# Performance work log

Measured on AMD Instinct MI355X. Metric: run time of the kernel, lower is better.

The kernel has to match this reference:

```python
import jax, jax.numpy as jnp
import numpy as np
from jax import lax

# config (matches init_kwargs)
HEADS = 4
KD2 = 256          # key_dim // 2
KNN = 16
BLOCK = 128        # knn * block_rate
COL = 512          # value_size // block
VALUE_SIZE = 65536 # key_num ** 2
D_OUT = 512
D_IN = 1024
QUERYDIM = HEADS * KD2  # 1024
KERNEL = 3


def setup_inputs() -> dict:
    key = jax.random.key(0)
    ks = jax.random.split(key, 8)
    B, T = 2, 2048
    return {
        "x": jax.random.normal(ks[0], (B, T, D_IN), dtype=jnp.float32),
        "conv_w": jax.random.normal(ks[1], (D_IN, 1, KERNEL), dtype=jnp.float32) * 0.1,
        "conv_b": jax.random.normal(ks[2], (D_IN,), dtype=jnp.float32) * 0.1,
        "lin_w": jax.random.normal(ks[3], (QUERYDIM, D_IN), dtype=jnp.float32) * (D_IN ** -0.5),
        "lin_b": jax.random.normal(ks[4], (QUERYDIM,), dtype=jnp.float32) * 0.1,
        "rowkeys": jax.random.normal(ks[5], (BLOCK, HEADS, KD2), dtype=jnp.float32) * (KD2 ** -0.5),
        "colkeys": jax.random.normal(ks[6], (COL, HEADS, KD2), dtype=jnp.float32) * (KD2 ** -0.5),
        "value_w": jax.random.normal(ks[7], (VALUE_SIZE, D_OUT), dtype=jnp.float32),
    }


def _forward(x, conv_w, conv_b, lin_w, lin_b, rowkeys, colkeys, value_w):
    B, T, C = x.shape
    # --- Querynet: causal depthwise conv1d + linear ---
    xt = jnp.transpose(x, (0, 2, 1))  # (B, C, T)
    y = lax.conv_general_dilated(
        xt, conv_w, window_strides=(1,), padding=[(KERNEL - 1, 0)],
        feature_group_count=C, dimension_numbers=("NCH", "OIH", "NCH"))
    y = y + conv_b[None, :, None]
    y = jnp.transpose(y, (0, 2, 1))                     # (B, T, C)
    query = y @ lin_w.T + lin_b                         # (B, T, querydim)
    # torch: query.view(B, heads, T, key_dim//2) -- raw C-order reshape
    q = query.reshape(B, HEADS, T, KD2)
    # --- block_wise_choice.get_indices ---
    score = jnp.einsum("bhtd,ehd->bhte", q, rowkeys)    # (B,H,T,block)
    col_scores = jnp.einsum("bhtd,chd->bhtc", q, colkeys)  # (B,H,T,col)
    score_col, idx_col = lax.top_k(col_scores, 1)       # (B,H,T,1)
    base = jnp.arange(BLOCK, dtype=jnp.int32)
    indices = base[None, None, None, :] * COL + idx_col  # (B,H,T,block)
    score = score + score_col                            # broadcast add
    # torch .view(B,H,-1,T): raw C-order reshape mixing tokens and blocks
    score = score.reshape(B, HEADS, BLOCK, T)
    indices = indices.reshape(B, HEADS, BLOCK, T)
    k = T * KNN // BLOCK
    score_top, dispatch = lax.top_k(score, k)            # (B,H,block,k), sorted desc
    idx_top = jnp.take_along_axis(indices, dispatch, axis=-1)
    score_r = score_top.reshape(B, BLOCK, -1)            # (B, block, H*k)
    idx_r = idx_top.reshape(B, BLOCK, -1)
    disp_r = dispatch.reshape(B, BLOCK, -1)
    # --- Memory_value: gather-weight-scatter ---
    gathered = value_w[idx_r]                            # (B, block, H*k, d)
    weighted = (gathered * score_r[..., None]).reshape(B, -1, D_OUT)
    flat_disp = disp_r.reshape(B, -1)                    # values in [0, T)
    out = jnp.zeros((B, T, D_OUT), dtype=weighted.dtype)
    out = out.at[jnp.arange(B)[:, None], flat_disp].add(weighted)
    return out


def reference(x, conv_w, conv_b, lin_w, lin_b, rowkeys, colkeys, value_w):
    return _forward(x, conv_w, conv_b, lin_w, lin_b, rowkeys, colkeys, value_w)
```

## Files before the change

### kernel.cpp

```cpp
#include <hip/hip_runtime.h>

constexpr int Bc   = 2;
constexpr int Tc   = 2048;
constexpr int Cc   = 1024;
constexpr int QDc  = 1024;
constexpr int Hc   = 4;
constexpr int KD2c = 256;
constexpr int BLKc = 128;
constexpr int COLc = 512;
constexpr int DOUTc= 512;
constexpr int KSELc= 256;
constexpr int NKEYS= BLKc + COLc;
constexpr int NBINS= Bc * Tc;
constexpr int NSEL = Bc * Hc * BLKc * KSELc;

typedef short bf16x8 __attribute__((ext_vector_type(8)));
typedef float f32x4  __attribute__((ext_vector_type(4)));

__device__ __forceinline__ unsigned short f2bf(float f) {
    unsigned u = __float_as_uint(f);
    u += 0x7FFFu + ((u >> 16) & 1u);
    return (unsigned short)(u >> 16);
}
__device__ __forceinline__ float bf2f(unsigned short h) {
    return __uint_as_float((unsigned)h << 16);
}
__device__ __forceinline__ void splitbf3(float f, unsigned short* h,
                                         unsigned short* m, unsigned short* l) {
    unsigned short hh = f2bf(f);
    float r1 = f - bf2f(hh);
    unsigned short mm = f2bf(r1);
    float r2 = r1 - bf2f(mm);
    *h = hh; *m = mm; *l = f2bf(r2);
}

__device__ __forceinline__ void gld_lds16(const void* g, void* l) {
    __builtin_amdgcn_global_load_lds(
        (const __attribute__((address_space(1))) unsigned int*)g,
        (__attribute__((address_space(3))) unsigned int*)l, 16, 0, 0);
}

__global__ __launch_bounds__(256) void conv_kernel(
    const float* __restrict__ x, const float* __restrict__ cw,
    const float* __restrict__ cb, unsigned short* __restrict__ y1,
    unsigned short* __restrict__ y2, unsigned short* __restrict__ y3)
{
    int idx = blockIdx.x * 256 + threadIdx.x;
    int c = idx & (Cc - 1);
    int t = (idx >> 10) & (Tc - 1);
    int b = idx >> 21;
    float w0 = cw[c*3+0], w1 = cw[c*3+1], w2 = cw[c*3+2];
    const float* xb = x + (size_t)b * Tc * Cc;
    float acc = cb[c] + w2 * xb[(size_t)t*Cc + c];
    if (t >= 1) acc += w1 * xb[(size_t)(t-1)*Cc + c];
    if (t >= 2) acc += w0 * xb[(size_t)(t-2)*Cc + c];
    splitbf3(acc, &y1[idx], &y2[idx], &y3[idx]);
}

__global__ __launch_bounds__(256) void convw_kernel(
    const float* __restrict__ w, unsigned short* __restrict__ w1,
    unsigned short* __restrict__ w2, unsigned short* __restrict__ w3)
{
    int idx = blockIdx.x * 256 + threadIdx.x;
    splitbf3(w[idx], &w1[idx], &w2[idx], &w3[idx]);
}

__global__ __launch_bounds__(256) void convkeys_kernel(
    const float* __restrict__ rowkeys, const float* __restrict__ colkeys,
    unsigned short* __restrict__ k1, unsigned short* __restrict__ k2,
    unsigned short* __restrict__ k3)
{
    int bid = blockIdx.x;
    int h = bid / NKEYS, n = bid % NKEYS;
    int k = threadIdx.x;
    float v = (n < BLKc) ? rowkeys[((size_t)n*Hc + h)*KD2c + k]
                         : colkeys[((size_t)(n-BLKc)*Hc + h)*KD2c + k];
    size_t o = ((size_t)h*NKEYS + n)*KD2c + k;
    splitbf3(v, &k1[o], &k2[o], &k3[o]);
}

__device__ __forceinline__ void mfma_gemm_tile(
    const unsigned short* __restrict__ A1g, const unsigned short* __restrict__ A2g,
    const unsigned short* __restrict__ A3g, int lda,
    const unsigned short* __restrict__ B1g, const unsigned short* __restrict__ B2g,
    const unsigned short* __restrict__ B3g, int ldb,
    int K, int m0, int n0, char* lds, f32x4 acc[4][2])
{
    const int tid  = threadIdx.x;
    const int wave = tid >> 6, lane = tid & 63;
    const int wr = wave >> 2, wc = wave & 3;
    const int g = lane >> 4, r16 = lane & 15;

    int aoff[4], boff[2];
    #pragma unroll
    for (int i = 0; i < 4; i++) {
        int ra = wr*64 + i*16 + r16;
        aoff[i] = ra*64 + ((g ^ ((ra>>1)&3)) << 4);
    }
    #pragma unroll
    for (int j = 0; j < 2; j++) {
        int rb = wc*32 + j*16 + r16;
        boff[j] = rb*64 + ((g ^ ((rb>>1)&3)) << 4);
    }
    const int row0 = tid >> 2, kg0 = ((tid & 3) ^ ((row0>>1)&3)) * 8;
    char* d0 = lds + wave*1024;

#define STAGE(kc, bo) do {                                                 \
        size_t a0_ = (size_t)(m0+row0)*lda + (kc) + kg0;                   \
        size_t b0_ = (size_t)(n0+row0)*ldb + (kc) + kg0;                   \
        gld_lds16(A1g + a0_, d0 + (bo));                                   \
        gld_lds16(A2g + a0_, d0 + 8192 + (bo));                            \
        gld_lds16(A3g + a0_, d0 + 16384 + (bo));                           \
        gld_lds16(B1g + b0_, d0 + 24576 + (bo));                           \
        gld_lds16(B2g + b0_, d0 + 32768 + (bo));                           \
        gld_lds16(B3g + b0_, d0 + 40960 + (bo));                           \
    } while (0)

    auto compute = [&](int bo) {
        bf16x8 a1[4], a2[4], a3[4], b1[2], b2[2], b3[2];
        #pragma unroll
        for (int i = 0; i < 4; i++) {
            a1[i] = *(const bf16x8*)(lds + bo + aoff[i]);
            a2[i] = *(const bf16x8*)(lds + bo +  8192 + aoff[i]);
            a3[i] = *(const bf16x8*)(lds + bo + 16384 + aoff[i]);
        }
        #pragma unroll
        for (int j = 0; j < 2; j++) {
            b1[j] = *(const bf16x8*)(lds + bo + 24576 + boff[j]);
            b2[j] = *(const bf16x8*)(lds + bo + 32768 + boff[j]);
            b3[j] = *(const bf16x8*)(lds + bo + 40960 + boff[j]);
        }
        #pragma unroll
        for (int i = 0; i < 4; i++)
            #pragma unroll
            for (int j = 0; j < 2; j++) {
                acc[i][j] = __builtin_amdgcn_mfma_f32_16x16x32_bf16(a3[i], b1[j], acc[i][j], 0, 0, 0);
                acc[i][j] = __builtin_amdgcn_mfma_f32_16x16x32_bf16(a2[i], b2[j], acc[i][j], 0, 0, 0);
                acc[i][j] = __builtin_amdgcn_mfma_f32_16x16x32_bf16(a1[i], b3[j], acc[i][j], 0, 0, 0);
                acc[i][j] = __builtin_amdgcn_mfma_f32_16x16x32_bf16(a2[i], b1[j], acc[i][j], 0, 0, 0);
                acc[i][j] = __builtin_amdgcn_mfma_f32_16x16x32_bf16(a1[i], b2[j], acc[i][j], 0, 0, 0);
                acc[i][j] = __builtin_amdgcn_mfma_f32_16x16x32_bf16(a1[i], b1[j], acc[i][j], 0, 0, 0);
            }
    };

    const int NT = K / 32;
    STAGE(0, 0);
    int bo = 0;
    for (int t = 0; t < NT - 1; ++t) {
        STAGE((t+1)*32, bo ^ 49152);
        asm volatile("s_waitcnt vmcnt(6)" ::: "memory");
        __builtin_amdgcn_s_barrier();
        asm volatile("" ::: "memory");
        compute(bo);
        asm volatile("" ::: "memory");
        __builtin_amdgcn_s_barrier();
        bo ^= 49152;
    }
    asm volatile("s_waitcnt vmcnt(0)" ::: "memory");
    __builtin_amdgcn_s_barrier();
    asm volatile("" ::: "memory");
    compute(bo);
#undef STAGE
}

__global__ __launch_bounds__(512) void qgemm_kernel(
    const unsigned short* __restrict__ y1, const unsigned short* __restrict__ y2,
    const unsigned short* __restrict__ y3,
    const unsigned short* __restrict__ w1, const unsigned short* __restrict__ w2,
    const unsigned short* __restrict__ w3,
    const float* __restrict__ bias,
    unsigned short* __restrict__ q1, unsigned short* __restrict__ q2,
    unsigned short* __restrict__ q3)
{
    __shared__ char lds[98304];
    int l = blockIdx.x;
    int yb = (l & 7) * 4 + ((l >> 3) & 3);
    int xb = l >> 5;
    int m0 = yb * 128, n0 = xb * 128;
    f32x4 acc[4][2];
    #pragma unroll
    for (int i = 0; i < 4; i++)
        #pragma unroll
        for (int j = 0; j < 2; j++) acc[i][j] = (f32x4)0.f;
    mfma_gemm_tile(y1, y2, y3, Cc, w1, w2, w3, Cc, Cc, m0, n0, lds, acc);

    const int lane = threadIdx.x & 63, wave = threadIdx.x >> 6;
    const int wr = wave >> 2, wc = wave & 3;
    const int g = lane >> 4, r16 = lane & 15;
    #pragma unroll
    for (int i = 0; i < 4; i++)
        #pragma unroll
        for (int j = 0; j < 2; j++)
            #pragma unroll
            for (int reg = 0; reg < 4; reg++) {
                int m = m0 + wr*64 + i*16 + g*4 + reg;
                int n = n0 + wc*32 + j*16 + r16;
                float v = acc[i][j][reg] + bias[n];
                size_t o = (size_t)m * QDc + n;
                splitbf3(v, &q1[o], &q2[o], &q3[o]);
            }
}

__global__ __launch_bounds__(512) void sgemm_kernel(
    const unsigned short* __restrict__ q1, const unsigned short* __restrict__ q2,
    const unsigned short* __restrict__ q3,
    const unsigned short* __restrict__ k1, const unsigned short* __restrict__ k2,
    const unsigned short* __restrict__ k3,
    float* __restrict__ Ctmp)
{
    __shared__ char lds[98304];
    int l = blockIdx.x;
    int b4h = l & 7;
    int m5  = l >> 3;
    int xb  = m5 % 5;
    int yb  = m5 / 5;
    size_t qo = (size_t)b4h * (Tc * KD2c);
    size_t ko = (size_t)(b4h & 3) * (NKEYS * KD2c);
    int m0 = yb * 128, n0 = xb * 128;
    f32x4 acc[4][2];
    #pragma unroll
    for (int i = 0; i < 4; i++)
        #pragma unroll
        for (int j = 0; j < 2; j++) acc[i][j] = (f32x4)0.f;
    mfma_gemm_tile(q1+qo, q2+qo, q3+qo, KD2c, k1+ko, k2+ko, k3+ko, KD2c,
                   KD2c, m0, n0, lds, acc);

    const int lane = threadIdx.x & 63, wave = threadIdx.x >> 6;
    const int wr = wave >> 2, wc = wave & 3;
    const int g = lane >> 4, r16 = lane & 15;
    float* Cb = Ctmp + (size_t)b4h * Tc * NKEYS;
    #pragma unroll
    for (int i = 0; i < 4; i++)
        #pragma unroll
        for (int j = 0; j < 2; j++)
            #pragma unroll
            for (int reg = 0; reg < 4; reg++) {
                int m = m0 + wr*64 + i*16 + g*4 + reg;
                int n = n0 + wc*32 + j*16 + r16;
                Cb[(size_t)m * NKEYS + n] = acc[i][j][reg];
            }
}

__global__ __launch_bounds__(256) void colmax_kernel(
    const float* __restrict__ Ctmp, float* __restrict__ s, int* __restrict__ cidx)
{
    int rid = blockIdx.x * 4 + (threadIdx.x >> 6);
    int lane = threadIdx.x & 63;
    const float* row = Ctmp + (size_t)rid * NKEYS;
    float best = -3.4e38f; int bi = 0;
    #pragma unroll
    for (int i = 0; i < 8; i++) {
        int c = lane + i*64;
        float v = row[BLKc + c];
        if (v > best) { best = v; bi = c; }
    }
    #pragma unroll
    for (int off = 32; off > 0; off >>= 1) {
        float ov = __shfl_xor(best, off, 64);
        int   oi = __shfl_xor(bi,   off, 64);
        if (ov > best || (ov == best && oi < bi)) { best = ov; bi = oi; }
    }
    if (lane == 0) cidx[rid] = bi;
    #pragma unroll
    for (int e = lane; e < BLKc; e += 64)
        s[(size_t)rid*BLKc + e] = row[e] + best;
}

__global__ __launch_bounds__(256) void topk_kernel(
    const float* __restrict__ s, const int* __restrict__ cidx,
    int* __restrict__ tk_j, int* __restrict__ tk_vidx, float* __restrict__ tk_score)
{
    int wid  = (blockIdx.x << 2) + (threadIdx.x >> 6);
    int lane = threadIdx.x & 63;
    int batch = wid >> 7;
    int i = wid & 127;
    const float* srow = s + (size_t)batch * (Tc*BLKc) + (size_t)i * 2048;

    unsigned key[8][4];
    #pragma unroll
    for (int r = 0; r < 8; r++) {
        float4 v4 = *(const float4*)&srow[r*256 + lane*4];
        float vv[4] = {v4.x, v4.y, v4.z, v4.w};
        #pragma unroll
        for (int e = 0; e < 4; e++) {
            unsigned u = __float_as_uint(vv[e]);
            key[r][e] = (u >> 31) ? ~u : (u | 0x80000000u);
        }
    }

    unsigned lo = 0, hi = 0xFFFFFFFFu;
    while (lo < hi) {
        unsigned d = hi - lo;
        unsigned mid = lo + ((d >> 1) + (d & 1u));
        int cnt = 0;
        #pragma unroll
        for (int r = 0; r < 8; r++)
            #pragma unroll
            for (int e = 0; e < 4; e++)
                cnt += (key[r][e] >= mid) ? 1 : 0;
        #pragma unroll
        for (int off = 32; off > 0; off >>= 1) cnt += __shfl_xor(cnt, off, 64);
        if (cnt >= KSELc) lo = mid; else hi = mid - 1;
    }
    const unsigned thr = lo;

    int gcnt = 0, ecnt = 0;
    unsigned eqmask = 0;
    #pragma unroll
    for (int r = 0; r < 8; r++)
        #pragma unroll
        for (int e = 0; e < 4; e++) {
            gcnt += (key[r][e] > thr) ? 1 : 0;
            if (key[r][e] == thr) { eqmask |= (1u << (r*4+e)); ecnt++; }
        }

    int gpre = gcnt, epre = ecnt;
    #pragma unroll
    for (int off = 1; off < 64; off <<= 1) {
        int gv = __shfl_up(gpre, off, 64);
        int ev = __shfl_up(epre, off, 64);
        if (lane >= off) { gpre += gv; epre += ev; }
    }
    const int total_greater = __shfl(gpre, 63, 64);
    const int total_eq      = __shfl(epre, 63, 64);
    const int gbase = gpre - gcnt;
    const int ebase = epre - ecnt;
    const int need  = KSELc - total_greater;

    const size_t obase = (size_t)wid * KSELc;
    const int cbase = batch * Tc + i * 16;

    int rk = 0;
    #pragma unroll
    for (int r = 0; r < 8; r++)
        #pragma unroll
        for (int e = 0; e < 4; e++) {
            if (key[r][e] > thr) {
                int j = r*256 + lane*4 + e;
                unsigned u = key[r][e];
                float f = (u >> 31) ? __uint_as_float(u ^ 0x80000000u)
                                    : __uint_as_float(~u);
                size_t o = obase + gbase + rk;
                tk_j[o] = j;
                tk_vidx[o] = (j & 127) * COLc + cidx[cbase + (j >> 7)];
                tk_score[o] = f;
                rk++;
            }
        }

    if (need == total_eq) {
        int erk = 0;
        #pragma unroll
        for (int r = 0; r < 8; r++)
            #pragma unroll
            for (int e = 0; e < 4; e++) {
                if (key[r][e] == thr) {
                    int j = r*256 + lane*4 + e;
                    float f = (thr >> 31) ? __uint_as_float(thr ^ 0x80000000u)
                                          : __uint_as_float(~thr);
                    size_t o = obase + total_greater + ebase + erk;
                    tk_j[o] = j;
                    tk_vidx[o] = (j & 127) * COLc + cidx[cbase + (j >> 7)];
                    tk_score[o] = f;
                    erk++;
                }
            }
    } else {
        unsigned em = eqmask;
        int left = need;
        while (left > 0) {
            int myj = 0x7FFFFFFF;
            if (em) {
                int bit = __builtin_ctz(em);
                myj = (bit >> 2)*256 + lane*4 + (bit & 3);
            }
            int mn = myj;
            #pragma unroll
            for (int off = 32; off > 0; off >>= 1) mn = min(mn, __shfl_xor(mn, off, 64));
            if (myj == mn) {
                em &= em - 1;
                int j = mn;
                float f = (thr >> 31) ? __uint_as_float(thr ^ 0x80000000u)
                                      : __uint_as_float(~thr);
                size_t o = obase + (KSELc - left);
                tk_j[o] = j;
                tk_vidx[o] = (j & 127) * COLc + cidx[cbase + (j >> 7)];
                tk_score[o] = f;
            }
            left--;
        }
    }
}

__global__ __launch_bounds__(256) void zero_bins_kernel(int* __restrict__ p, int n)
{
    int i = blockIdx.x * 256 + threadIdx.x;
    if (i < n) p[i] = 0;
}

__global__ __launch_bounds__(256) void count_kernel(
    const int* __restrict__ tk_j, int* __restrict__ counts)
{
    int idx = blockIdx.x * 256 + threadIdx.x;
    int r = idx >> 8;
    int b = r >> 9;
    int j = tk_j[idx];
    atomicAdd(&counts[b * Tc + j], 1);
}

__global__ __launch_bounds__(256) void scan_kernel(
    const int* __restrict__ counts, int* __restrict__ offsets)
{
    __shared__ int part[256];
    int tid = threadIdx.x;
    int local[16];
    int sum = 0;
    #pragma unroll
    for (int k = 0; k < 16; k++) { local[k] = sum; sum += counts[tid*16 + k]; }
    part[tid] = sum;
    __syncthreads();
    for (int st = 1; st < 256; st <<= 1) {
        int v = (tid >= st) ? part[tid - st] : 0;
        __syncthreads();
        part[tid] += v;
        __syncthreads();
    }
    int base = (tid == 0) ? 0 : part[tid - 1];
    #pragma unroll
    for (int k = 0; k < 16; k++) offsets[tid*16 + k] = base + local[k];
    if (tid == 255) offsets[NBINS] = base + sum;
}

__global__ __launch_bounds__(256) void fill_kernel(
    const int* __restrict__ tk_j, const int* __restrict__ tk_vidx,
    const float* __restrict__ tk_score, const int* __restrict__ offsets,
    int* __restrict__ fillctr, int* __restrict__ bin_vidx,
    float* __restrict__ bin_score)
{
    int idx = blockIdx.x * 256 + threadIdx.x;
    int r = idx >> 8;
    int b = r >> 9;
    int bin = b * Tc + tk_j[idx];
    int pos = offsets[bin] + atomicAdd(&fillctr[bin], 1);
    bin_vidx[pos]  = tk_vidx[idx];
    bin_score[pos] = tk_score[idx];
}

__global__ __launch_bounds__(256) void gather_kernel(
    const int* __restrict__ offsets, const int* __restrict__ bin_vidx,
    const float* __restrict__ bin_score, const float* __restrict__ value_w,
    float* __restrict__ out)
{
    __shared__ int   svidx[512];
    __shared__ float sscore[512];
    int bin = blockIdx.x;
    int tid = threadIdx.x;
    int beg = offsets[bin], cnt = offsets[bin + 1] - beg;
    for (int n = tid; n < cnt; n += 256) {
        svidx[n]  = bin_vidx[beg + n];
        sscore[n] = bin_score[beg + n];
    }
    __syncthreads();

    const int c = tid * 2;
    float accx = 0.f, accy = 0.f;
    int n = 0;
    for (; n + 8 <= cnt; n += 8) {
        int vi[8]; float sc[8]; float2 vv[8];
        #pragma unroll
        for (int k = 0; k < 8; k++) { vi[k] = svidx[n+k]; sc[k] = sscore[n+k]; }
        #pragma unroll
        for (int k = 0; k < 8; k++)
            vv[k] = *(const float2*)&value_w[(size_t)vi[k] * DOUTc + c];
        #pragma unroll
        for (int k = 0; k < 8; k++) { accx += sc[k]*vv[k].x; accy += sc[k]*vv[k].y; }
    }
    for (; n < cnt; n++) {
        int v = svidx[n]; float sc = sscore[n];
        float2 a = *(const float2*)&value_w[(size_t)v * DOUTc + c];
        accx += sc*a.x; accy += sc*a.y;
    }
    float2 res; res.x = accx; res.y = accy;
    *(float2*)&out[(size_t)bin * DOUTc + c] = res;
}

extern "C" void kernel_launch(void* const* d_in, const int* in_sizes, int n_in,
                              void* d_out, int out_size, void* d_ws, size_t ws_size,
                              hipStream_t stream)
{
    const float* x       = (const float*)d_in[0];
    const float* conv_w  = (const float*)d_in[1];
    const float* conv_b  = (const float*)d_in[2];
    const float* lin_w   = (const float*)d_in[3];
    const float* lin_b   = (const float*)d_in[4];
    const float* rowkeys = (const float*)d_in[5];
    const float* colkeys = (const float*)d_in[6];
    const float* value_w = (const float*)d_in[7];
    float* out = (float*)d_out;

    constexpr size_t MB = 1024*1024;
    char* w = (char*)d_ws;
    float*          Ctmp = (float*)(w);
    unsigned short* y1   = (unsigned short*)(w);
    unsigned short* y2   = (unsigned short*)(w +  8*MB);
    unsigned short* y3   = (unsigned short*)(w + 16*MB);
    unsigned short* w1   = (unsigned short*)(w + 24*MB);
    unsigned short* w2   = (unsigned short*)(w + 26*MB);
    unsigned short* w3   = (unsigned short*)(w + 28*MB);
    unsigned short* q1   = (unsigned short*)(w + 40*MB);
    unsigned short* q2   = (unsigned short*)(w + 48*MB);
    unsigned short* q3   = (unsigned short*)(w + 56*MB);
    unsigned short* k1   = (unsigned short*)(w + 64*MB);
    unsigned short* k2   = (unsigned short*)(w + 66*MB);
    unsigned short* k3   = (unsigned short*)(w + 68*MB);
    float*          s    = (float*)(w + 70*MB);
    int*            cidx = (int*)  (w + 78*MB);
    int*            tk_j = (int*)  (w + 79*MB);
    int*            tk_v = (int*)  (w + 80*MB);
    float*          tk_s = (float*)(w + 81*MB);
    int*            counts    = (int*)  (w + 82*MB);
    int*            offsets   = (int*)  (w + 82*MB + 32768);
    int*            fillctr   = (int*)  (w + 82*MB + 65536);
    int*            bin_vidx  = (int*)  (w + 82*MB + 131072);
    float*          bin_score = (float*)(w + 82*MB + 131072 + 1048576);

    conv_kernel<<<(Bc*Tc*Cc)/256, 256, 0, stream>>>(x, conv_w, conv_b, y1, y2, y3);
    convw_kernel<<<(QDc*Cc)/256, 256, 0, stream>>>(lin_w, w1, w2, w3);
    convkeys_kernel<<<Hc*NKEYS, 256, 0, stream>>>(rowkeys, colkeys, k1, k2, k3);
    qgemm_kernel<<<256, 512, 0, stream>>>(
        y1, y2, y3, w1, w2, w3, lin_b, q1, q2, q3);
    sgemm_kernel<<<640, 512, 0, stream>>>(
        q1, q2, q3, k1, k2, k3, Ctmp);
    colmax_kernel<<<(Bc*Hc*Tc)/4, 256, 0, stream>>>(Ctmp, s, cidx);
    topk_kernel<<<Bc*Hc*BLKc/4, 256, 0, stream>>>(s, cidx, tk_j, tk_v, tk_s);
    zero_bins_kernel<<<(96*1024/4 + 255)/256, 256, 0, stream>>>(counts, 96*1024/4);
    count_kernel<<<NSEL/256, 256, 0, stream>>>(tk_j, counts);
    scan_kernel<<<1, 256, 0, stream>>>(counts, offsets);
    fill_kernel<<<NSEL/256, 256, 0, stream>>>(tk_j, tk_v, tk_s, offsets,
                                              fillctr, bin_vidx, bin_score);
    gather_kernel<<<NBINS, 256, 0, stream>>>(offsets, bin_vidx, bin_score,
                                             value_w, out);
}
```

Before: 223.2 us.

## Bucket selections by value row slab and accumulate in LDS per block-row

Replaces the per-output-token gather (each token reading its selected value_w rows from global memory) with a bucketed scheme keyed by value-row slab. Each of the 256 workgroups stages 32-row chunks of value_w into LDS and scatters weighted contributions into a 32x512 LDS accumulator covering all output tokens that share its block index e. Results are flushed to the output with atomicAdd, which requires a new zero-fill kernel for the output. The aim is to read each value_w row once instead of once per selection. The cost is 128KB of LDS per workgroup, so occupancy is limited to one workgroup, only 256 workgroups run, and floating-point atomics make summation order nondeterministic.

```diff
diff --git a/kernel.cpp b/kernel.cpp
--- a/kernel.cpp
+++ b/kernel.cpp
@@ -13,6 +13,7 @@
 constexpr int NKEYS= BLKc + COLc;
 constexpr int NBINS= Bc * Tc;
 constexpr int NSEL = Bc * Hc * BLKc * KSELc;
+constexpr int NBUCK= 128 * 16;
 
 typedef short bf16x8 __attribute__((ext_vector_type(8)));
 typedef float f32x4  __attribute__((ext_vector_type(4)));
@@ -398,25 +399,32 @@
     if (i < n) p[i] = 0;
 }
 
-__global__ __launch_bounds__(256) void count_kernel(
-    const int* __restrict__ tk_j, int* __restrict__ counts)
+__global__ __launch_bounds__(256) void zero_out_kernel(float4* __restrict__ p, int n4)
+{
+    int i = blockIdx.x * 256 + threadIdx.x;
+    if (i < n4) p[i] = float4{0.f, 0.f, 0.f, 0.f};
+}
+
+__global__ __launch_bounds__(256) void count2_kernel(
+    const int* __restrict__ tk_j, const int* __restrict__ tk_vidx,
+    int* __restrict__ counts2)
 {
     int idx = blockIdx.x * 256 + threadIdx.x;
-    int r = idx >> 8;
-    int b = r >> 9;
     int j = tk_j[idx];
-    atomicAdd(&counts[b * Tc + j], 1);
-}
-
-__global__ __launch_bounds__(256) void scan_kernel(
-    const int* __restrict__ counts, int* __restrict__ offsets)
+    int ci = tk_vidx[idx] & 511;
+    int bucket = (j & 127) * 16 + (ci >> 5);
+    atomicAdd(&counts2[bucket], 1);
+}
+
+__global__ __launch_bounds__(256) void scan2_kernel(
+    const int* __restrict__ counts2, int* __restrict__ boff2)
 {
     __shared__ int part[256];
     int tid = threadIdx.x;
-    int local[16];
+    int local[8];
     int sum = 0;
     #pragma unroll
-    for (int k = 0; k < 16; k++) { local[k] = sum; sum += counts[tid*16 + k]; }
+    for (int k = 0; k < 8; k++) { local[k] = sum; sum += counts2[tid*8 + k]; }
     part[tid] = sum;
     __syncthreads();
     for (int st = 1; st < 256; st <<= 1) {
@@ -427,61 +435,103 @@
     }
     int base = (tid == 0) ? 0 : part[tid - 1];
     #pragma unroll
-    for (int k = 0; k < 16; k++) offsets[tid*16 + k] = base + local[k];
-    if (tid == 255) offsets[NBINS] = base + sum;
-}
-
-__global__ __launch_bounds__(256) void fill_kernel(
+    for (int k = 0; k < 8; k++) boff2[tid*8 + k] = base + local[k];
+    if (tid == 255) boff2[NBUCK] = base + sum;
+}
+
+__global__ __launch_bounds__(256) void fill2_kernel(
     const int* __restrict__ tk_j, const int* __restrict__ tk_vidx,
-    const float* __restrict__ tk_score, const int* __restrict__ offsets,
-    int* __restrict__ fillctr, int* __restrict__ bin_vidx,
-    float* __restrict__ bin_score)
+    const float* __restrict__ tk_score, const int* __restrict__ boff2,
+    int* __restrict__ fc2, int* __restrict__ bpay, float* __restrict__ bsc)
 {
     int idx = blockIdx.x * 256 + threadIdx.x;
     int r = idx >> 8;
     int b = r >> 9;
-    int bin = b * Tc + tk_j[idx];
-    int pos = offsets[bin] + atomicAdd(&fillctr[bin], 1);
-    bin_vidx[pos]  = tk_vidx[idx];
-    bin_score[pos] = tk_score[idx];
-}
-
-__global__ __launch_bounds__(256) void gather_kernel(
-    const int* __restrict__ offsets, const int* __restrict__ bin_vidx,
-    const float* __restrict__ bin_score, const float* __restrict__ value_w,
+    int j = tk_j[idx];
+    int ci = tk_vidx[idx] & 511;
+    int e = j & 127;
+    int bucket = e * 16 + (ci >> 5);
+    int lb = b * 16 + (j >> 7);
+    int rl = ci & 31;
+    int pos = boff2[bucket] + atomicAdd(&fc2[bucket], 1);
+    bpay[pos] = (lb << 5) | rl;
+    bsc[pos]  = tk_score[idx];
+}
+
+__global__ __launch_bounds__(256) void gather_slab_kernel(
+    const int* __restrict__ boff2, const int* __restrict__ bpay,
+    const float* __restrict__ bsc, const float* __restrict__ value_w,
     float* __restrict__ out)
 {
-    __shared__ int   svidx[512];
-    __shared__ float sscore[512];
-    int bin = blockIdx.x;
-    int tid = threadIdx.x;
-    int beg = offsets[bin], cnt = offsets[bin + 1] - beg;
-    for (int n = tid; n < cnt; n += 256) {
-        svidx[n]  = bin_vidx[beg + n];
-        sscore[n] = bin_score[beg + n];
-    }
+    __shared__ float vch[32 * 512];
+    __shared__ float acc[32 * 512];
+    __shared__ int   epay[512];
+    __shared__ float esc[512];
+
+    const int e   = blockIdx.x >> 1;
+    const int par = blockIdx.x & 1;
+    const int tid = threadIdx.x;
+    const int wave = tid >> 6, lane = tid & 63;
+
+    #pragma unroll
+    for (int k = 0; k < 64; k++) acc[k * 256 + tid] = 0.f;
     __syncthreads();
 
     const int c = tid * 2;
-    float accx = 0.f, accy = 0.f;
-    int n = 0;
-    for (; n + 8 <= cnt; n += 8) {
-        int vi[8]; float sc[8]; float2 vv[8];
-        #pragma unroll
-        for (int k = 0; k < 8; k++) { vi[k] = svidx[n+k]; sc[k] = sscore[n+k]; }
-        #pragma unroll
-        for (int k = 0; k < 8; k++)
-            vv[k] = *(const float2*)&value_w[(size_t)vi[k] * DOUTc + c];
-        #pragma unroll
-        for (int k = 0; k < 8; k++) { accx += sc[k]*vv[k].x; accy += sc[k]*vv[k].y; }
-    }
-    for (; n < cnt; n++) {
-        int v = svidx[n]; float sc = sscore[n];
-        float2 a = *(const float2*)&value_w[(size_t)v * DOUTc + c];
-        accx += sc*a.x; accy += sc*a.y;
-    }
-    float2 res; res.x = accx; res.y = accy;
-    *(float2*)&out[(size_t)bin * DOUTc + c] = res;
+
+    for (int chunk = par; chunk < 16; chunk += 2) {
+        const float* src = value_w + ((size_t)(e * 512 + chunk * 32)) * DOUTc;
+        char* dst = (char*)vch + wave * 1024;
+        #pragma unroll
+        for (int it = 0; it < 16; it++)
+            gld_lds16((const char*)src + it*4096 + wave*1024 + lane*16,
+                      dst + it*4096);
+        asm volatile("s_waitcnt vmcnt(0)" ::: "memory");
+        __syncthreads();
+
+        int bucket = e * 16 + chunk;
+        int beg = boff2[bucket], end = boff2[bucket + 1];
+        for (int tile = beg; tile < end; tile += 512) {
+            int tcnt = min(end - tile, 512);
+            if (tid < tcnt)        { epay[tid]     = bpay[tile+tid];     esc[tid]     = bsc[tile+tid]; }
+            if (tid + 256 < tcnt)  { epay[tid+256] = bpay[tile+tid+256]; esc[tid+256] = bsc[tile+tid+256]; }
+            __syncthreads();
+            int n = 0;
+            for (; n + 2 <= tcnt; n += 2) {
+                int p0 = epay[n],   p1 = epay[n+1];
+                float s0 = esc[n],  s1 = esc[n+1];
+                int a0 = (p0 >> 5) * 512 + c, r0 = (p0 & 31) * 512 + c;
+                int a1 = (p1 >> 5) * 512 + c, r1 = (p1 & 31) * 512 + c;
+                float2 v0 = *(float2*)&vch[r0];
+                float2 v1 = *(float2*)&vch[r1];
+                float2 x0 = *(float2*)&acc[a0];
+                x0.x += s0 * v0.x; x0.y += s0 * v0.y;
+                *(float2*)&acc[a0] = x0;
+                float2 x1 = *(float2*)&acc[a1];
+                x1.x += s1 * v1.x; x1.y += s1 * v1.y;
+                *(float2*)&acc[a1] = x1;
+            }
+            for (; n < tcnt; n++) {
+                int p = epay[n]; float sc = esc[n];
+                int a = (p >> 5) * 512 + c, rl = (p & 31) * 512 + c;
+                float2 v = *(float2*)&vch[rl];
+                float2 x = *(float2*)&acc[a];
+                x.x += sc * v.x; x.y += sc * v.y;
+                *(float2*)&acc[a] = x;
+            }
+            __syncthreads();
+        }
+        __syncthreads();
+    }
+
+    #pragma unroll
+    for (int lb = 0; lb < 32; lb++) {
+        int bin = (lb >> 4) * Tc + (lb & 15) * 128 + e;
+        float2 v = *(float2*)&acc[lb * 512 + c];
+        float* orow = out + (size_t)bin * DOUTc + c;
+        atomicAdd(&orow[0], v.x);
+        atomicAdd(&orow[1], v.y);
+    }
 }
 
 extern "C" void kernel_launch(void* const* d_in, const int* in_sizes, int n_in,
@@ -518,12 +568,14 @@
     int*            tk_j = (int*)  (w + 79*MB);
     int*            tk_v = (int*)  (w + 80*MB);
     float*          tk_s = (float*)(w + 81*MB);
-    int*            counts    = (int*)  (w + 82*MB);
-    int*            offsets   = (int*)  (w + 82*MB + 32768);
-    int*            fillctr   = (int*)  (w + 82*MB + 65536);
-    int*            bin_vidx  = (int*)  (w + 82*MB + 131072);
-    float*          bin_score = (float*)(w + 82*MB + 131072 + 1048576);
-
+    int*            counts2 = (int*)  (w + 82*MB);
+    int*            boff2   = (int*)  (w + 82*MB + 16384);
+    int*            fc2     = (int*)  (w + 82*MB + 32768);
+    int*            bpay    = (int*)  (w + 82*MB + 131072);
+    float*          bsc     = (float*)(w + 82*MB + 131072 + 1048576);
+
+    zero_bins_kernel<<<(96*1024/4 + 255)/256, 256, 0, stream>>>(counts2, 96*1024/4);
+    zero_out_kernel<<<(out_size/4 + 255)/256, 256, 0, stream>>>((float4*)out, out_size/4);
     conv_kernel<<<(Bc*Tc*Cc)/256, 256, 0, stream>>>(x, conv_w, conv_b, y1, y2, y3);
     convw_kernel<<<(QDc*Cc)/256, 256, 0, stream>>>(lin_w, w1, w2, w3);
     convkeys_kernel<<<Hc*NKEYS, 256, 0, stream>>>(rowkeys, colkeys, k1, k2, k3);
@@ -533,11 +585,9 @@
         q1, q2, q3, k1, k2, k3, Ctmp);
     colmax_kernel<<<(Bc*Hc*Tc)/4, 256, 0, stream>>>(Ctmp, s, cidx);
     topk_kernel<<<Bc*Hc*BLKc/4, 256, 0, stream>>>(s, cidx, tk_j, tk_v, tk_s);
-    zero_bins_kernel<<<(96*1024/4 + 255)/256, 256, 0, stream>>>(counts, 96*1024/4);
-    count_kernel<<<NSEL/256, 256, 0, stream>>>(tk_j, counts);
-    scan_kernel<<<1, 256, 0, stream>>>(counts, offsets);
-    fill_kernel<<<NSEL/256, 256, 0, stream>>>(tk_j, tk_v, tk_s, offsets,
-                                              fillctr, bin_vidx, bin_score);
-    gather_kernel<<<NBINS, 256, 0, stream>>>(offsets, bin_vidx, bin_score,
-                                             value_w, out);
-}
+    count2_kernel<<<NSEL/256, 256, 0, stream>>>(tk_j, tk_v, counts2);
+    scan2_kernel<<<1, 256, 0, stream>>>(counts2, boff2);
+    fill2_kernel<<<NSEL/256, 256, 0, stream>>>(tk_j, tk_v, tk_s, boff2,
+                                               fc2, bpay, bsc);
+    gather_slab_kernel<<<256, 256, 0, stream>>>(boff2, bpay, bsc, value_w, out);
+}
```

Result: slower. 363.3 us (+62.8%).
